# Optimization experiments

Hardware: AMD Instinct MI355X
Metric: run time of the kernel (lower is better)

Reference implementation:

```python
import jax, jax.numpy as jnp
import numpy as np

EMBED = 1024
HEADS = 16
HEAD_DIM = EMBED // HEADS
SCALING = HEAD_DIM ** -0.5
R = 16
LORA_SCALE = 32.0 / R  # alpha / r
NEG = jnp.finfo(jnp.float32).min


def lora_linear(x, W, A, B):
    # y = x @ W.T + (x @ A.T) @ B.T * scale   (LinearLora, bias=False)
    return x @ W.T + ((x @ A.T) @ B.T) * LORA_SCALE


def setup_inputs() -> dict:
    key = jax.random.key(0)
    ks = jax.random.split(key, 14)
    B, T, D = 1, 4096, EMBED
    hidden_states = jax.random.normal(ks[0], (B, T, D), jnp.float32)
    # causal additive mask (bsz, 1, tgt, src): 0 on/below diag, dtype-min above
    i = jnp.arange(T)
    causal = jnp.where(i[:, None] >= i[None, :], 0.0, NEG).astype(jnp.float32)
    attention_mask = jnp.broadcast_to(causal, (B, 1, T, T))
    s = 0.02
    def w(k, shape):
        return jax.random.normal(k, shape, jnp.float32) * s
    return dict(
        hidden_states=hidden_states,
        attention_mask=attention_mask,
        Wq=w(ks[1], (D, D)), Wk=w(ks[2], (D, D)), Wv=w(ks[3], (D, D)), Wo=w(ks[4], (D, D)),
        Aq=w(ks[5], (R, D)), Bq=jnp.zeros((D, R), jnp.float32) + w(ks[6], (D, R)),
        Ak=w(ks[7], (R, D)), Bk=w(ks[8], (D, R)),
        Av=w(ks[9], (R, D)), Bv=w(ks[10], (D, R)),
        Ao=w(ks[11], (R, D)), Bo=w(ks[12], (D, R)),
    )


def reference(hidden_states, attention_mask, Wq, Wk, Wv, Wo,
              Aq, Bq, Ak, Bk, Av, Bv, Ao, Bo):
    bsz, tgt_len, _ = hidden_states.shape
    H, Hd = HEADS, HEAD_DIM

    q = lora_linear(hidden_states, Wq, Aq, Bq) * SCALING
    k = lora_linear(hidden_states, Wk, Ak, Bk)
    v = lora_linear(hidden_states, Wv, Av, Bv)

    # (b, t, H, Hd)
    q = q.reshape(bsz, tgt_len, H, Hd)
    k = k.reshape(bsz, tgt_len, H, Hd)
    v = v.reshape(bsz, tgt_len, H, Hd)

    # scores (b, H, t, s)
    attn = jnp.einsum('bthd,bshd->bhts', q, k)
    attn = attn + attention_mask
    attn = jnp.maximum(attn, NEG)
    attn = jax.nn.softmax(attn, axis=-1)  # dropout p=0 / eval mode

    out = jnp.einsum('bhts,bshd->bthd', attn, v)
    out = out.reshape(bsz, tgt_len, H * Hd)
    out = lora_linear(out, Wo, Ao, Bo)
    return out
```

## Files before the change

kernel.cpp:

```cpp
#include <hip/hip_runtime.h>
#include <cmath>
#include <cstdint>

typedef unsigned short u16;
typedef __attribute__((ext_vector_type(8))) __bf16 bf16x8;
typedef __attribute__((ext_vector_type(4))) __bf16 bf16x4;
typedef __attribute__((ext_vector_type(4))) short s16x4;
typedef __attribute__((ext_vector_type(4))) float f32x4;

__device__ __forceinline__ u16 f2bf(float f) {
    union { float f; unsigned u; } v; v.f = f;
    unsigned r = v.u + 0x7fffu + ((v.u >> 16) & 1u);
    return (u16)(r >> 16);
}

__device__ __forceinline__ void gload_lds(const u16* g, u16* l) {
    __builtin_amdgcn_global_load_lds((__attribute__((address_space(1))) void*)g,
                                     (__attribute__((address_space(3))) void*)l,
                                     16, 0, 0);
}

__device__ __forceinline__ f32x4 mfma16(s16x4 a, s16x4 b, f32x4 c) {
#if __has_builtin(__builtin_amdgcn_mfma_f32_16x16x16bf16_1k)
    return __builtin_amdgcn_mfma_f32_16x16x16bf16_1k(a, b, c, 0, 0, 0);
#else
    asm("v_mfma_f32_16x16x16_bf16 %0, %1, %2, %3"
        : "=v"(c) : "v"(a), "v"(b), "0"(c));
    return c;
#endif
}

__global__ __launch_bounds__(256) void prep_all(
        const float* __restrict__ X,
        const float* __restrict__ Wq, const float* __restrict__ Wk,
        const float* __restrict__ Wv, const float* __restrict__ Wo,
        const float* __restrict__ Aq, const float* __restrict__ Bq,
        const float* __restrict__ Ak, const float* __restrict__ Bk,
        const float* __restrict__ Av, const float* __restrict__ Bv,
        const float* __restrict__ Ao, const float* __restrict__ Bo,
        u16* __restrict__ Wqkv, u16* __restrict__ Wob, u16* __restrict__ Xb) {
    const int p = blockIdx.y;
    const int idx = blockIdx.x * 256 + threadIdx.x;
    if (p == 4) {
        float4 v = ((const float4*)X)[idx];
        ushort4 o;
        o.x = f2bf(v.x); o.y = f2bf(v.y); o.z = f2bf(v.z); o.w = f2bf(v.w);
        ((ushort4*)Xb)[idx] = o;
        return;
    }
    const int n = idx >> 10, d = idx & 1023;
    const float* W; const float* A; const float* B;
    switch (p) {
        case 0: W = Wq; A = Aq; B = Bq; break;
        case 1: W = Wk; A = Ak; B = Bk; break;
        case 2: W = Wv; A = Av; B = Bv; break;
        default: W = Wo; A = Ao; B = Bo; break;
    }
    float lora = 0.f;
#pragma unroll
    for (int r = 0; r < 16; r++) lora += B[n * 16 + r] * A[r * 1024 + d];
    float v = W[idx] + 2.0f * lora;
    if (p == 0) v *= 0.125f * 1.44269504088896340736f;
    if (p < 3) Wqkv[(size_t)p * 1048576 + idx] = f2bf(v);
    else       Wob[idx] = f2bf(v);
}

template <bool F32OUT>
__global__ __launch_bounds__(256) void gemm_bt(const u16* __restrict__ A,
                                               const u16* __restrict__ B,
                                               void* __restrict__ C, int ldc) {
    __shared__ __align__(16) u16 As[128 * 32];
    __shared__ __align__(16) u16 Bs[128 * 32];
    const int tid = threadIdx.x;
    const int lane = tid & 63, wave = tid >> 6;
    const int quad = lane >> 4, l16 = lane & 15;
    const int wm = (wave >> 1) * 64, wn = (wave & 1) * 64;
    const size_t m0 = (size_t)blockIdx.y * 128, n0 = (size_t)blockIdx.x * 128;
    const u16* Ap = A + m0 * 1024;
    const u16* Bp = B + n0 * 1024;
    f32x4 acc[4][4] = {};
    for (int k0 = 0; k0 < 1024; k0 += 32) {
#pragma unroll
        for (int hh = 0; hh < 2; hh++) {
            int c = tid + hh * 256;
            int row = c >> 2, cp = (c & 3) * 8;
            gload_lds(Ap + (size_t)row * 1024 + k0 + cp, As + c * 8);
            gload_lds(Bp + (size_t)row * 1024 + k0 + cp, Bs + c * 8);
        }
        __syncthreads();
        bf16x8 af[4], bfr[4];
#pragma unroll
        for (int i = 0; i < 4; i++) {
            af[i]  = *(const bf16x8*)(As + (wm + i * 16 + l16) * 32 + quad * 8);
            bfr[i] = *(const bf16x8*)(Bs + (wn + i * 16 + l16) * 32 + quad * 8);
        }
#pragma unroll
        for (int mi = 0; mi < 4; mi++)
#pragma unroll
            for (int ni = 0; ni < 4; ni++)
                acc[mi][ni] = __builtin_amdgcn_mfma_f32_16x16x32_bf16(
                        af[mi], bfr[ni], acc[mi][ni], 0, 0, 0);
        __syncthreads();
    }
#pragma unroll
    for (int mi = 0; mi < 4; mi++)
#pragma unroll
        for (int ni = 0; ni < 4; ni++)
#pragma unroll
            for (int r = 0; r < 4; r++) {
                size_t row = m0 + wm + mi * 16 + quad * 4 + r;
                size_t col = n0 + wn + ni * 16 + l16;
                if (F32OUT) ((float*)C)[row * ldc + col] = acc[mi][ni][r];
                else        ((u16*)C)[row * ldc + col] = f2bf(acc[mi][ni][r]);
            }
}

template <bool F32OUT>
__global__ __launch_bounds__(256) void gemm_bt64(const u16* __restrict__ A,
                                                 const u16* __restrict__ B,
                                                 void* __restrict__ C, int ldc) {
    __shared__ __align__(16) u16 As[64 * 32];
    __shared__ __align__(16) u16 Bs[128 * 32];
    const int tid = threadIdx.x;
    const int lane = tid & 63, wave = tid >> 6;
    const int quad = lane >> 4, l16 = lane & 15;
    const int wm = (wave >> 1) * 32, wn = (wave & 1) * 64;
    const size_t m0 = (size_t)blockIdx.y * 64, n0 = (size_t)blockIdx.x * 128;
    const u16* Ap = A + m0 * 1024;
    const u16* Bp = B + n0 * 1024;
    f32x4 acc[2][4] = {};
    for (int k0 = 0; k0 < 1024; k0 += 32) {
        {
            int c = tid;
            int row = c >> 2, cp = (c & 3) * 8;
            gload_lds(Ap + (size_t)row * 1024 + k0 + cp, As + c * 8);
#pragma unroll
            for (int hh = 0; hh < 2; hh++) {
                int b = hh * 256 + tid;
                int brow = b >> 2, bcp = (b & 3) * 8;
                gload_lds(Bp + (size_t)brow * 1024 + k0 + bcp, Bs + b * 8);
            }
        }
        __syncthreads();
        bf16x8 af[2], bfr[4];
#pragma unroll
        for (int i = 0; i < 2; i++)
            af[i] = *(const bf16x8*)(As + (wm + i * 16 + l16) * 32 + quad * 8);
#pragma unroll
        for (int i = 0; i < 4; i++)
            bfr[i] = *(const bf16x8*)(Bs + (wn + i * 16 + l16) * 32 + quad * 8);
#pragma unroll
        for (int mi = 0; mi < 2; mi++)
#pragma unroll
            for (int ni = 0; ni < 4; ni++)
                acc[mi][ni] = __builtin_amdgcn_mfma_f32_16x16x32_bf16(
                        af[mi], bfr[ni], acc[mi][ni], 0, 0, 0);
        __syncthreads();
    }
#pragma unroll
    for (int mi = 0; mi < 2; mi++)
#pragma unroll
        for (int ni = 0; ni < 4; ni++)
#pragma unroll
            for (int r = 0; r < 4; r++) {
                size_t row = m0 + wm + mi * 16 + quad * 4 + r;
                size_t col = n0 + wn + ni * 16 + l16;
                if (F32OUT) ((float*)C)[row * ldc + col] = acc[mi][ni][r];
                else        ((u16*)C)[row * ldc + col] = f2bf(acc[mi][ni][r]);
            }
}

__global__ __launch_bounds__(256) void transpose_v(const u16* __restrict__ Y,
                                                   u16* __restrict__ Vt) {
    __shared__ u16 tile[64][68];
    const int dv0 = blockIdx.x * 64;
    const int t0  = blockIdx.y * 64;
    const int tid = threadIdx.x;
#pragma unroll
    for (int p = 0; p < 4; p++) {
        int pos = tid + p * 256;
        int row = pos >> 4;
        int c4  = (pos & 15) * 4;
        ushort4 v = *(const ushort4*)(Y + (size_t)(t0 + row) * 3072 + 2048 + dv0 + c4);
        tile[row][c4 + 0] = v.x; tile[row][c4 + 1] = v.y;
        tile[row][c4 + 2] = v.z; tile[row][c4 + 3] = v.w;
    }
    __syncthreads();
#pragma unroll
    for (int p = 0; p < 4; p++) {
        int pos = tid + p * 256;
        int orow = pos >> 4;
        int oc4  = (pos & 15) * 4;
        ushort4 o;
        o.x = tile[oc4 + 0][orow]; o.y = tile[oc4 + 1][orow];
        o.z = tile[oc4 + 2][orow]; o.w = tile[oc4 + 3][orow];
        *(ushort4*)(Vt + (size_t)(dv0 + orow) * 4096 + t0 + oc4) = o;
    }
}

__global__ __launch_bounds__(256) void flash_attn(const u16* __restrict__ Y,
                                                  const u16* __restrict__ Vt,
                                                  u16* __restrict__ O) {
    __shared__ __align__(16) u16 lds[16384];
    const int tid = threadIdx.x;
    const int wave = tid >> 6, lane = tid & 63;
    const int quad = lane >> 4, l16 = lane & 15;
    const int h = blockIdx.x & 15;
    const int pr = blockIdx.x >> 4;
    const u16* Kbase = Y + 1024 + h * 64;
    const u16* Vbase = Vt + (size_t)(h * 64) * 4096;
    const int xsw = l16 & 7;

#pragma unroll 1
    for (int ph = 0; ph < 2; ph++) {
        const int p = ph ? (63 - pr) : pr;
        const int q0w = p * 64 + wave * 16;
        const int nT = p + 1;

        bf16x8 qf[2];
#pragma unroll
        for (int kf = 0; kf < 2; kf++)
            qf[kf] = *(const bf16x8*)(Y + (size_t)(q0w + l16) * 3072
                                        + h * 64 + kf * 32 + quad * 8);

        f32x4 oaccT[4] = {};
        float l_i = 0.f;

#pragma unroll
        for (int pp = 0; pp < 2; pp++) {
            int c = pp * 256 + tid;
            int row = c >> 3, cg = (c & 7) ^ (row & 7);
            gload_lds(Kbase + (size_t)row * 3072 + cg * 8, lds + c * 8);
            gload_lds(Vbase + (size_t)row * 4096 + cg * 8, lds + 4096 + c * 8);
        }

#pragma unroll 1
        for (int t = 0; t < nT; t++) {
            const int s0 = t * 64;
            u16* Ks = lds + (t & 1) * 8192;
            u16* Vs = Ks + 4096;
            asm volatile("s_waitcnt vmcnt(0)" ::: "memory");
            __syncthreads();

            if (t + 1 < nT) {
                u16* Kn = lds + ((t + 1) & 1) * 8192;
                const int sn = s0 + 64;
#pragma unroll
                for (int pp = 0; pp < 2; pp++) {
                    int c = pp * 256 + tid;
                    int row = c >> 3, cg = (c & 7) ^ (row & 7);
                    gload_lds(Kbase + (size_t)(sn + row) * 3072 + cg * 8, Kn + c * 8);
                    gload_lds(Vbase + (size_t)row * 4096 + sn + cg * 8, Kn + 4096 + c * 8);
                }
            }

            bf16x8 kfr[4][2];
#pragma unroll
            for (int ni = 0; ni < 4; ni++) {
                int row = ni * 16 + l16;
                kfr[ni][0] = *(const bf16x8*)(Ks + row * 64 + ((quad) ^ xsw) * 8);
                kfr[ni][1] = *(const bf16x8*)(Ks + row * 64 + ((4 + quad) ^ xsw) * 8);
            }
            f32x4 sacc[4] = {};
#pragma unroll
            for (int ni = 0; ni < 4; ni++) {
                sacc[ni] = __builtin_amdgcn_mfma_f32_16x16x32_bf16(
                        kfr[ni][0], qf[0], sacc[ni], 0, 0, 0);
                sacc[ni] = __builtin_amdgcn_mfma_f32_16x16x32_bf16(
                        kfr[ni][1], qf[1], sacc[ni], 0, 0, 0);
            }
            s16x4 vfr[4][4];
#pragma unroll
            for (int nj = 0; nj < 4; nj++) {
                int row = nj * 16 + l16;
#pragma unroll
                for (int ni = 0; ni < 4; ni++) {
                    int cc = ni * 2 + (quad >> 1);
                    vfr[nj][ni] = *(const s16x4*)(Vs + row * 64 + (cc ^ xsw) * 8
                                                     + (quad & 1) * 4);
                }
            }

            if (t == nT - 1) {
                const int qg = q0w + l16;
#pragma unroll
                for (int ni = 0; ni < 4; ni++)
#pragma unroll
                    for (int r = 0; r < 4; r++) {
                        int sg = s0 + ni * 16 + quad * 4 + r;
                        if (sg > qg) sacc[ni][r] = -INFINITY;
                    }
            }
            float rs = 0.f;
            s16x4 pf[4];
#pragma unroll
            for (int ni = 0; ni < 4; ni++) {
                f32x4 pe;
#pragma unroll
                for (int r = 0; r < 4; r++) {
                    pe[r] = __builtin_amdgcn_exp2f(sacc[ni][r]);
                    rs += pe[r];
                }
                bf16x4 tt = { (__bf16)pe[0], (__bf16)pe[1],
                              (__bf16)pe[2], (__bf16)pe[3] };
                pf[ni] = __builtin_bit_cast(s16x4, tt);
            }
            rs += __shfl_xor(rs, 16);
            rs += __shfl_xor(rs, 32);
            l_i += rs;

#pragma unroll
            for (int nj = 0; nj < 4; nj++)
#pragma unroll
                for (int ni = 0; ni < 4; ni++)
                    oaccT[nj] = mfma16(vfr[nj][ni], pf[ni], oaccT[nj]);
        }

        __syncthreads();
        u16* scr = lds + wave * 1152;
        {
            float inv = 1.0f / l_i;
#pragma unroll
            for (int nj = 0; nj < 4; nj++) {
                bf16x4 t4 = { (__bf16)(oaccT[nj][0] * inv),
                              (__bf16)(oaccT[nj][1] * inv),
                              (__bf16)(oaccT[nj][2] * inv),
                              (__bf16)(oaccT[nj][3] * inv) };
                *(s16x4*)(scr + l16 * 72 + nj * 16 + quad * 4) =
                        __builtin_bit_cast(s16x4, t4);
            }
        }
        asm volatile("s_waitcnt lgkmcnt(0)" ::: "memory");
#pragma unroll
        for (int pp = 0; pp < 2; pp++) {
            int row = pp * 8 + (lane >> 3);
            int seg = (lane & 7) * 8;
            bf16x8 d = *(const bf16x8*)(scr + row * 72 + seg);
            *(bf16x8*)(O + (size_t)(p * 64 + wave * 16 + row) * 1024
                         + h * 64 + seg) = d;
        }
        __syncthreads();
    }
}


extern "C" void kernel_launch(void* const* d_in, const int* in_sizes, int n_in,
                              void* d_out, int out_size, void* d_ws, size_t ws_size,
                              hipStream_t stream) {
    const float* X  = (const float*)d_in[0];
    const float* Wq = (const float*)d_in[2];
    const float* Wk = (const float*)d_in[3];
    const float* Wv = (const float*)d_in[4];
    const float* Wo = (const float*)d_in[5];
    const float* Aq = (const float*)d_in[6];
    const float* Bq = (const float*)d_in[7];
    const float* Ak = (const float*)d_in[8];
    const float* Bk = (const float*)d_in[9];
    const float* Av = (const float*)d_in[10];
    const float* Bv = (const float*)d_in[11];
    const float* Ao = (const float*)d_in[12];
    const float* Bo = (const float*)d_in[13];

    char* ws = (char*)d_ws;
    u16* Xb   = (u16*)(ws);
    u16* Wqkv = (u16*)(ws + (8u  << 20));
    u16* Wob  = (u16*)(ws + (14u << 20));
    u16* Y    = (u16*)(ws + (16u << 20));
    u16* Vt   = (u16*)(ws + (40u << 20));
    u16* Ob   = (u16*)(ws + (48u << 20));

    prep_all<<<dim3(4096, 5), 256, 0, stream>>>(X, Wq, Wk, Wv, Wo, Aq, Bq, Ak, Bk,
                                                Av, Bv, Ao, Bo, Wqkv, Wob, Xb);
    gemm_bt<false><<<dim3(24, 32), 256, 0, stream>>>(Xb, Wqkv, Y, 3072);
    transpose_v<<<dim3(16, 64), 256, 0, stream>>>(Y, Vt);
    flash_attn<<<dim3(512), 256, 0, stream>>>(Y, Vt, Ob);
    gemm_bt64<true><<<dim3(8, 64), 256, 0, stream>>>(Ob, Wob, d_out, 1024);
}
```

Measured before the change: 279.7 us.

## Deepen GEMM K-tiles with swizzled LDS and split attention into one-tile blocks

Both projection GEMMs now stage 64-wide K slices instead of 32, with an XOR swizzle on the LDS layout to avoid bank conflicts, which halves the number of barrier-separated iterations. Flash attention no longer pairs two query tiles per block. It launches 1024 single-tile blocks, ordered so the long causal rows are scheduled first, and loads V fragments before the score MFMAs. Occupancy hints are added via launch bounds. The trade-offs are larger LDS use per GEMM block and more, smaller attention blocks in place of the built-in balanced pairing.

```diff
diff --git a/kernel.cpp b/kernel.cpp
--- a/kernel.cpp
+++ b/kernel.cpp
@@ -66,11 +66,11 @@
 }
 
 template <bool F32OUT>
-__global__ __launch_bounds__(256) void gemm_bt(const u16* __restrict__ A,
-                                               const u16* __restrict__ B,
-                                               void* __restrict__ C, int ldc) {
-    __shared__ __align__(16) u16 As[128 * 32];
-    __shared__ __align__(16) u16 Bs[128 * 32];
+__global__ __launch_bounds__(256, 3) void gemm_bt(const u16* __restrict__ A,
+                                                  const u16* __restrict__ B,
+                                                  void* __restrict__ C, int ldc) {
+    __shared__ __align__(16) u16 As[128 * 64];
+    __shared__ __align__(16) u16 Bs[128 * 64];
     const int tid = threadIdx.x;
     const int lane = tid & 63, wave = tid >> 6;
     const int quad = lane >> 4, l16 = lane & 15;
@@ -78,28 +78,35 @@
     const size_t m0 = (size_t)blockIdx.y * 128, n0 = (size_t)blockIdx.x * 128;
     const u16* Ap = A + m0 * 1024;
     const u16* Bp = B + n0 * 1024;
+    const int xsw = l16 & 7;
     f32x4 acc[4][4] = {};
-    for (int k0 = 0; k0 < 1024; k0 += 32) {
-#pragma unroll
-        for (int hh = 0; hh < 2; hh++) {
+    for (int k0 = 0; k0 < 1024; k0 += 64) {
+#pragma unroll
+        for (int hh = 0; hh < 4; hh++) {
             int c = tid + hh * 256;
-            int row = c >> 2, cp = (c & 3) * 8;
-            gload_lds(Ap + (size_t)row * 1024 + k0 + cp, As + c * 8);
-            gload_lds(Bp + (size_t)row * 1024 + k0 + cp, Bs + c * 8);
-        }
-        __syncthreads();
-        bf16x8 af[4], bfr[4];
-#pragma unroll
-        for (int i = 0; i < 4; i++) {
-            af[i]  = *(const bf16x8*)(As + (wm + i * 16 + l16) * 32 + quad * 8);
-            bfr[i] = *(const bf16x8*)(Bs + (wn + i * 16 + l16) * 32 + quad * 8);
-        }
-#pragma unroll
-        for (int mi = 0; mi < 4; mi++)
-#pragma unroll
-            for (int ni = 0; ni < 4; ni++)
-                acc[mi][ni] = __builtin_amdgcn_mfma_f32_16x16x32_bf16(
-                        af[mi], bfr[ni], acc[mi][ni], 0, 0, 0);
+            int row = c >> 3, cg = (c & 7) ^ (row & 7);
+            gload_lds(Ap + (size_t)row * 1024 + k0 + cg * 8, As + c * 8);
+            gload_lds(Bp + (size_t)row * 1024 + k0 + cg * 8, Bs + c * 8);
+        }
+        asm volatile("s_waitcnt vmcnt(0)" ::: "memory");
+        __syncthreads();
+#pragma unroll
+        for (int kf = 0; kf < 2; kf++) {
+            bf16x8 af[4], bfr[4];
+#pragma unroll
+            for (int i = 0; i < 4; i++) {
+                af[i]  = *(const bf16x8*)(As + (wm + i * 16 + l16) * 64
+                                             + ((kf * 4 + quad) ^ xsw) * 8);
+                bfr[i] = *(const bf16x8*)(Bs + (wn + i * 16 + l16) * 64
+                                             + ((kf * 4 + quad) ^ xsw) * 8);
+            }
+#pragma unroll
+            for (int mi = 0; mi < 4; mi++)
+#pragma unroll
+                for (int ni = 0; ni < 4; ni++)
+                    acc[mi][ni] = __builtin_amdgcn_mfma_f32_16x16x32_bf16(
+                            af[mi], bfr[ni], acc[mi][ni], 0, 0, 0);
+        }
         __syncthreads();
     }
 #pragma unroll
@@ -116,11 +123,11 @@
 }
 
 template <bool F32OUT>
-__global__ __launch_bounds__(256) void gemm_bt64(const u16* __restrict__ A,
-                                                 const u16* __restrict__ B,
-                                                 void* __restrict__ C, int ldc) {
-    __shared__ __align__(16) u16 As[64 * 32];
-    __shared__ __align__(16) u16 Bs[128 * 32];
+__global__ __launch_bounds__(256, 3) void gemm_bt64(const u16* __restrict__ A,
+                                                    const u16* __restrict__ B,
+                                                    void* __restrict__ C, int ldc) {
+    __shared__ __align__(16) u16 As[64 * 64];
+    __shared__ __align__(16) u16 Bs[128 * 64];
     const int tid = threadIdx.x;
     const int lane = tid & 63, wave = tid >> 6;
     const int quad = lane >> 4, l16 = lane & 15;
@@ -128,33 +135,41 @@
     const size_t m0 = (size_t)blockIdx.y * 64, n0 = (size_t)blockIdx.x * 128;
     const u16* Ap = A + m0 * 1024;
     const u16* Bp = B + n0 * 1024;
+    const int xsw = l16 & 7;
     f32x4 acc[2][4] = {};
-    for (int k0 = 0; k0 < 1024; k0 += 32) {
-        {
-            int c = tid;
-            int row = c >> 2, cp = (c & 3) * 8;
-            gload_lds(Ap + (size_t)row * 1024 + k0 + cp, As + c * 8);
-#pragma unroll
-            for (int hh = 0; hh < 2; hh++) {
-                int b = hh * 256 + tid;
-                int brow = b >> 2, bcp = (b & 3) * 8;
-                gload_lds(Bp + (size_t)brow * 1024 + k0 + bcp, Bs + b * 8);
-            }
-        }
-        __syncthreads();
-        bf16x8 af[2], bfr[4];
-#pragma unroll
-        for (int i = 0; i < 2; i++)
-            af[i] = *(const bf16x8*)(As + (wm + i * 16 + l16) * 32 + quad * 8);
-#pragma unroll
-        for (int i = 0; i < 4; i++)
-            bfr[i] = *(const bf16x8*)(Bs + (wn + i * 16 + l16) * 32 + quad * 8);
-#pragma unroll
-        for (int mi = 0; mi < 2; mi++)
-#pragma unroll
-            for (int ni = 0; ni < 4; ni++)
-                acc[mi][ni] = __builtin_amdgcn_mfma_f32_16x16x32_bf16(
-                        af[mi], bfr[ni], acc[mi][ni], 0, 0, 0);
+    for (int k0 = 0; k0 < 1024; k0 += 64) {
+#pragma unroll
+        for (int hh = 0; hh < 2; hh++) {
+            int c = tid + hh * 256;
+            int row = c >> 3, cg = (c & 7) ^ (row & 7);
+            gload_lds(Ap + (size_t)row * 1024 + k0 + cg * 8, As + c * 8);
+        }
+#pragma unroll
+        for (int hh = 0; hh < 4; hh++) {
+            int c = tid + hh * 256;
+            int row = c >> 3, cg = (c & 7) ^ (row & 7);
+            gload_lds(Bp + (size_t)row * 1024 + k0 + cg * 8, Bs + c * 8);
+        }
+        asm volatile("s_waitcnt vmcnt(0)" ::: "memory");
+        __syncthreads();
+#pragma unroll
+        for (int kf = 0; kf < 2; kf++) {
+            bf16x8 af[2], bfr[4];
+#pragma unroll
+            for (int i = 0; i < 2; i++)
+                af[i] = *(const bf16x8*)(As + (wm + i * 16 + l16) * 64
+                                            + ((kf * 4 + quad) ^ xsw) * 8);
+#pragma unroll
+            for (int i = 0; i < 4; i++)
+                bfr[i] = *(const bf16x8*)(Bs + (wn + i * 16 + l16) * 64
+                                             + ((kf * 4 + quad) ^ xsw) * 8);
+#pragma unroll
+            for (int mi = 0; mi < 2; mi++)
+#pragma unroll
+                for (int ni = 0; ni < 4; ni++)
+                    acc[mi][ni] = __builtin_amdgcn_mfma_f32_16x16x32_bf16(
+                            af[mi], bfr[ni], acc[mi][ni], 0, 0, 0);
+        }
         __syncthreads();
     }
 #pragma unroll
@@ -198,148 +213,150 @@
     }
 }
 
-__global__ __launch_bounds__(256) void flash_attn(const u16* __restrict__ Y,
-                                                  const u16* __restrict__ Vt,
-                                                  u16* __restrict__ O) {
+__global__ __launch_bounds__(256, 4) void flash_attn(const u16* __restrict__ Y,
+                                                     const u16* __restrict__ Vt,
+                                                     u16* __restrict__ O) {
     __shared__ __align__(16) u16 lds[16384];
     const int tid = threadIdx.x;
     const int wave = tid >> 6, lane = tid & 63;
     const int quad = lane >> 4, l16 = lane & 15;
-    const int h = blockIdx.x & 15;
-    const int pr = blockIdx.x >> 4;
+    const int bid = blockIdx.x;
+    const int rr = bid & 255, j = bid >> 8;
+    const int b = rr >> 4, h = rr & 15;
+    int p;
+    switch (j) { case 0:  p = 63 - b; break;
+                 case 1:  p = 32 + b; break;
+                 case 2:  p = 31 - b; break;
+                 default: p = b;      break; }
+    const int q0 = p * 64;
+    const int q0w = q0 + wave * 16;
+    const int nT = p + 1;
     const u16* Kbase = Y + 1024 + h * 64;
     const u16* Vbase = Vt + (size_t)(h * 64) * 4096;
     const int xsw = l16 & 7;
 
+    bf16x8 qf[2];
+#pragma unroll
+    for (int kf = 0; kf < 2; kf++)
+        qf[kf] = *(const bf16x8*)(Y + (size_t)(q0w + l16) * 3072
+                                    + h * 64 + kf * 32 + quad * 8);
+
+    f32x4 oaccT[4] = {};
+    float l_i = 0.f;
+
+#pragma unroll
+    for (int pp = 0; pp < 2; pp++) {
+        int c = pp * 256 + tid;
+        int row = c >> 3, cg = (c & 7) ^ (row & 7);
+        gload_lds(Kbase + (size_t)row * 3072 + cg * 8, lds + c * 8);
+        gload_lds(Vbase + (size_t)row * 4096 + cg * 8, lds + 4096 + c * 8);
+    }
+
 #pragma unroll 1
-    for (int ph = 0; ph < 2; ph++) {
-        const int p = ph ? (63 - pr) : pr;
-        const int q0w = p * 64 + wave * 16;
-        const int nT = p + 1;
-
-        bf16x8 qf[2];
-#pragma unroll
-        for (int kf = 0; kf < 2; kf++)
-            qf[kf] = *(const bf16x8*)(Y + (size_t)(q0w + l16) * 3072
-                                        + h * 64 + kf * 32 + quad * 8);
-
-        f32x4 oaccT[4] = {};
-        float l_i = 0.f;
-
-#pragma unroll
-        for (int pp = 0; pp < 2; pp++) {
-            int c = pp * 256 + tid;
-            int row = c >> 3, cg = (c & 7) ^ (row & 7);
-            gload_lds(Kbase + (size_t)row * 3072 + cg * 8, lds + c * 8);
-            gload_lds(Vbase + (size_t)row * 4096 + cg * 8, lds + 4096 + c * 8);
-        }
-
-#pragma unroll 1
-        for (int t = 0; t < nT; t++) {
-            const int s0 = t * 64;
-            u16* Ks = lds + (t & 1) * 8192;
-            u16* Vs = Ks + 4096;
-            asm volatile("s_waitcnt vmcnt(0)" ::: "memory");
-            __syncthreads();
-
-            if (t + 1 < nT) {
-                u16* Kn = lds + ((t + 1) & 1) * 8192;
-                const int sn = s0 + 64;
-#pragma unroll
-                for (int pp = 0; pp < 2; pp++) {
-                    int c = pp * 256 + tid;
-                    int row = c >> 3, cg = (c & 7) ^ (row & 7);
-                    gload_lds(Kbase + (size_t)(sn + row) * 3072 + cg * 8, Kn + c * 8);
-                    gload_lds(Vbase + (size_t)row * 4096 + sn + cg * 8, Kn + 4096 + c * 8);
+    for (int t = 0; t < nT; t++) {
+        const int s0 = t * 64;
+        u16* Ks = lds + (t & 1) * 8192;
+        u16* Vs = Ks + 4096;
+        asm volatile("s_waitcnt vmcnt(0)" ::: "memory");
+        __syncthreads();
+
+        if (t + 1 < nT) {
+            u16* Kn = lds + ((t + 1) & 1) * 8192;
+            const int sn = s0 + 64;
+#pragma unroll
+            for (int pp = 0; pp < 2; pp++) {
+                int c = pp * 256 + tid;
+                int row = c >> 3, cg = (c & 7) ^ (row & 7);
+                gload_lds(Kbase + (size_t)(sn + row) * 3072 + cg * 8, Kn + c * 8);
+                gload_lds(Vbase + (size_t)row * 4096 + sn + cg * 8, Kn + 4096 + c * 8);
+            }
+        }
+
+        bf16x8 kfr[4][2];
+#pragma unroll
+        for (int ni = 0; ni < 4; ni++) {
+            int row = ni * 16 + l16;
+            kfr[ni][0] = *(const bf16x8*)(Ks + row * 64 + ((quad) ^ xsw) * 8);
+            kfr[ni][1] = *(const bf16x8*)(Ks + row * 64 + ((4 + quad) ^ xsw) * 8);
+        }
+        s16x4 vfr[4][4];
+#pragma unroll
+        for (int nj = 0; nj < 4; nj++) {
+            int row = nj * 16 + l16;
+#pragma unroll
+            for (int ni = 0; ni < 4; ni++) {
+                int cc = ni * 2 + (quad >> 1);
+                vfr[nj][ni] = *(const s16x4*)(Vs + row * 64 + (cc ^ xsw) * 8
+                                                 + (quad & 1) * 4);
+            }
+        }
+        asm volatile("s_waitcnt lgkmcnt(0)" ::: "memory");
+
+        f32x4 sacc[4] = {};
+#pragma unroll
+        for (int ni = 0; ni < 4; ni++) {
+            sacc[ni] = __builtin_amdgcn_mfma_f32_16x16x32_bf16(
+                    kfr[ni][0], qf[0], sacc[ni], 0, 0, 0);
+            sacc[ni] = __builtin_amdgcn_mfma_f32_16x16x32_bf16(
+                    kfr[ni][1], qf[1], sacc[ni], 0, 0, 0);
+        }
+
+        if (t == nT - 1) {
+            const int qg = q0w + l16;
+#pragma unroll
+            for (int ni = 0; ni < 4; ni++)
+#pragma unroll
+                for (int r = 0; r < 4; r++) {
+                    int sg = s0 + ni * 16 + quad * 4 + r;
+                    if (sg > qg) sacc[ni][r] = -INFINITY;
                 }
-            }
-
-            bf16x8 kfr[4][2];
-#pragma unroll
-            for (int ni = 0; ni < 4; ni++) {
-                int row = ni * 16 + l16;
-                kfr[ni][0] = *(const bf16x8*)(Ks + row * 64 + ((quad) ^ xsw) * 8);
-                kfr[ni][1] = *(const bf16x8*)(Ks + row * 64 + ((4 + quad) ^ xsw) * 8);
-            }
-            f32x4 sacc[4] = {};
-#pragma unroll
-            for (int ni = 0; ni < 4; ni++) {
-                sacc[ni] = __builtin_amdgcn_mfma_f32_16x16x32_bf16(
-                        kfr[ni][0], qf[0], sacc[ni], 0, 0, 0);
-                sacc[ni] = __builtin_amdgcn_mfma_f32_16x16x32_bf16(
-                        kfr[ni][1], qf[1], sacc[ni], 0, 0, 0);
-            }
-            s16x4 vfr[4][4];
-#pragma unroll
-            for (int nj = 0; nj < 4; nj++) {
-                int row = nj * 16 + l16;
-#pragma unroll
-                for (int ni = 0; ni < 4; ni++) {
-                    int cc = ni * 2 + (quad >> 1);
-                    vfr[nj][ni] = *(const s16x4*)(Vs + row * 64 + (cc ^ xsw) * 8
-                                                     + (quad & 1) * 4);
-                }
-            }
-
-            if (t == nT - 1) {
-                const int qg = q0w + l16;
-#pragma unroll
-                for (int ni = 0; ni < 4; ni++)
-#pragma unroll
-                    for (int r = 0; r < 4; r++) {
-                        int sg = s0 + ni * 16 + quad * 4 + r;
-                        if (sg > qg) sacc[ni][r] = -INFINITY;
-                    }
-            }
-            float rs = 0.f;
-            s16x4 pf[4];
-#pragma unroll
-            for (int ni = 0; ni < 4; ni++) {
-                f32x4 pe;
-#pragma unroll
-                for (int r = 0; r < 4; r++) {
-                    pe[r] = __builtin_amdgcn_exp2f(sacc[ni][r]);
-                    rs += pe[r];
-                }
-                bf16x4 tt = { (__bf16)pe[0], (__bf16)pe[1],
-                              (__bf16)pe[2], (__bf16)pe[3] };
-                pf[ni] = __builtin_bit_cast(s16x4, tt);
-            }
-            rs += __shfl_xor(rs, 16);
-            rs += __shfl_xor(rs, 32);
-            l_i += rs;
-
-#pragma unroll
-            for (int nj = 0; nj < 4; nj++)
-#pragma unroll
-                for (int ni = 0; ni < 4; ni++)
-                    oaccT[nj] = mfma16(vfr[nj][ni], pf[ni], oaccT[nj]);
-        }
-
-        __syncthreads();
-        u16* scr = lds + wave * 1152;
-        {
-            float inv = 1.0f / l_i;
-#pragma unroll
-            for (int nj = 0; nj < 4; nj++) {
-                bf16x4 t4 = { (__bf16)(oaccT[nj][0] * inv),
-                              (__bf16)(oaccT[nj][1] * inv),
-                              (__bf16)(oaccT[nj][2] * inv),
-                              (__bf16)(oaccT[nj][3] * inv) };
-                *(s16x4*)(scr + l16 * 72 + nj * 16 + quad * 4) =
-                        __builtin_bit_cast(s16x4, t4);
-            }
-        }
-        asm volatile("s_waitcnt lgkmcnt(0)" ::: "memory");
-#pragma unroll
-        for (int pp = 0; pp < 2; pp++) {
-            int row = pp * 8 + (lane >> 3);
-            int seg = (lane & 7) * 8;
-            bf16x8 d = *(const bf16x8*)(scr + row * 72 + seg);
-            *(bf16x8*)(O + (size_t)(p * 64 + wave * 16 + row) * 1024
-                         + h * 64 + seg) = d;
-        }
-        __syncthreads();
+        }
+        float rs = 0.f;
+        s16x4 pf[4];
+#pragma unroll
+        for (int ni = 0; ni < 4; ni++) {
+            f32x4 pe;
+#pragma unroll
+            for (int r = 0; r < 4; r++) {
+                pe[r] = __builtin_amdgcn_exp2f(sacc[ni][r]);
+                rs += pe[r];
+            }
+            bf16x4 tt = { (__bf16)pe[0], (__bf16)pe[1],
+                          (__bf16)pe[2], (__bf16)pe[3] };
+            pf[ni] = __builtin_bit_cast(s16x4, tt);
+        }
+        rs += __shfl_xor(rs, 16);
+        rs += __shfl_xor(rs, 32);
+        l_i += rs;
+
+#pragma unroll
+        for (int nj = 0; nj < 4; nj++)
+#pragma unroll
+            for (int ni = 0; ni < 4; ni++)
+                oaccT[nj] = mfma16(vfr[nj][ni], pf[ni], oaccT[nj]);
+    }
+
+    __syncthreads();
+    u16* scr = lds + wave * 1152;
+    {
+        float inv = 1.0f / l_i;
+#pragma unroll
+        for (int nj = 0; nj < 4; nj++) {
+            bf16x4 t4 = { (__bf16)(oaccT[nj][0] * inv),
+                          (__bf16)(oaccT[nj][1] * inv),
+                          (__bf16)(oaccT[nj][2] * inv),
+                          (__bf16)(oaccT[nj][3] * inv) };
+            *(s16x4*)(scr + l16 * 72 + nj * 16 + quad * 4) =
+                    __builtin_bit_cast(s16x4, t4);
+        }
+    }
+    asm volatile("s_waitcnt lgkmcnt(0)" ::: "memory");
+#pragma unroll
+    for (int pp = 0; pp < 2; pp++) {
+        int row = pp * 8 + (lane >> 3);
+        int seg = (lane & 7) * 8;
+        bf16x8 d = *(const bf16x8*)(scr + row * 72 + seg);
+        *(bf16x8*)(O + (size_t)(q0w + row) * 1024 + h * 64 + seg) = d;
     }
 }
 
@@ -373,6 +390,6 @@
                                                 Av, Bv, Ao, Bo, Wqkv, Wob, Xb);
     gemm_bt<false><<<dim3(24, 32), 256, 0, stream>>>(Xb, Wqkv, Y, 3072);
     transpose_v<<<dim3(16, 64), 256, 0, stream>>>(Y, Vt);
-    flash_attn<<<dim3(512), 256, 0, stream>>>(Y, Vt, Ob);
+    flash_attn<<<dim3(1024), 256, 0, stream>>>(Y, Vt, Ob);
     gemm_bt64<true><<<dim3(8, 64), 256, 0, stream>>>(Ob, Wob, d_out, 1024);
 }
```

Measured after the change: 257.3 us. 8.0% less time.
